# Kernel optimization log

Measured on AMD Instinct MI355X. Metric: run time of the kernel, lower is better.

## Reference

```python
import jax, jax.numpy as jnp
import numpy as np

N, IN_FT, OUT_FT = 10000, 512, 256


def setup_inputs() -> dict:
    key = jax.random.key(0)
    k1, k2, k3 = jax.random.split(key, 3)
    feat = jax.random.normal(k1, (N, IN_FT), dtype=jnp.float32)
    adj = jax.random.uniform(k2, (N, N), dtype=jnp.float32)  # nonneg edge weights
    W = jax.random.normal(k3, (IN_FT, OUT_FT), dtype=jnp.float32) * 0.05
    conv_bias = jnp.zeros((OUT_FT,), dtype=jnp.float32)
    extra_bias = jnp.zeros((OUT_FT,), dtype=jnp.float32)
    return {"feat": feat, "adj": adj, "W": W,
            "conv_bias": conv_bias, "extra_bias": extra_bias}


def reference(feat, adj, W, conv_bias, extra_bias):
    n = adj.shape[0]
    idx = jnp.arange(n)
    # gcn_norm: fill_diag(adj, 1.0) -> self loops with weight 1 on the diagonal
    A_hat = adj.at[idx, idx].set(1.0)  # [N, N]
    deg = A_hat.sum(axis=1)            # row degree
    dinv = jnp.where(deg > 0, jax.lax.rsqrt(deg), 0.0)  # D^-1/2
    # linear transform first (standard GCNConv order), then normalized aggregation
    h = feat @ W                                   # [N, OUT_FT]
    # D^-1/2 A_hat D^-1/2 h, fused as row/col scalings to avoid a second NxN buffer
    agg = dinv[:, None] * (A_hat @ (dinv[:, None] * h))
    out = agg + conv_bias + extra_bias
    return jax.nn.relu(out)
```

## Files before the change

### kernel.cpp

```cpp
#include <hip/hip_runtime.h>

#define NROW 10000
#define NF 256
#define KF 512
#define MP 10048
#define NTILES 157
#define CCH 2512

typedef __attribute__((ext_vector_type(8))) short short8x;
typedef __attribute__((ext_vector_type(4))) float f32x4;

__device__ __forceinline__ unsigned int bf16rne(float f){
  unsigned int u = __builtin_bit_cast(unsigned int, f);
  u += 0x7fffu + ((u >> 16) & 1u);
  return u >> 16;
}

__global__ void k_zero(float4* __restrict__ p){
  p[blockIdx.x * 256 + threadIdx.x] = make_float4(0.f, 0.f, 0.f, 0.f);
}

__global__ __launch_bounds__(256) void k_prep(const float* __restrict__ adj,
        unsigned short* __restrict__ adjb, float* __restrict__ degp){
  int t = threadIdx.x;
  int lane = t & 63;
  int row = blockIdx.x * 4 + (t >> 6);
  int cy = blockIdx.y;
  int c0 = cy * CCH;
  int limit = (cy < 3) ? 628 : 616;
  const f32x4* src = (const f32x4*)(adj + (size_t)row * NROW + c0);
  unsigned short* dst = adjb + (size_t)row * MP + c0;
  const f32x4 zero4 = {0.f, 0.f, 0.f, 0.f};

  f32x4 v[5][2];
  #pragma unroll
  for (int it = 0; it < 4; ++it){
    int fi = it * 128 + lane * 2;
    v[it][0] = __builtin_nontemporal_load(src + fi);
    v[it][1] = __builtin_nontemporal_load(src + fi + 1);
  }
  {
    int fi = 512 + lane * 2;
    v[4][0] = (fi     < limit) ? __builtin_nontemporal_load(src + fi)     : zero4;
    v[4][1] = (fi + 1 < limit) ? __builtin_nontemporal_load(src + fi + 1) : zero4;
  }

  float s = 0.f;
  #pragma unroll
  for (int it = 0; it < 5; ++it){
    int fi0 = it * 128 + lane * 2;
    uint4 o;
    #pragma unroll
    for (int j = 0; j < 2; ++j){
      f32x4 w = v[it][j];
      int gc = c0 + (fi0 + j) * 4;
      if (row == gc    ) w[0] = 1.f;
      if (row == gc + 1) w[1] = 1.f;
      if (row == gc + 2) w[2] = 1.f;
      if (row == gc + 3) w[3] = 1.f;
      s += (w[0] + w[1]) + (w[2] + w[3]);
      unsigned int lo = bf16rne(w[0]) | (bf16rne(w[1]) << 16);
      unsigned int hi = bf16rne(w[2]) | (bf16rne(w[3]) << 16);
      if (j == 0){ o.x = lo; o.y = hi; } else { o.z = lo; o.w = hi; }
    }
    if (it < 4 || fi0 < 628)
      *(uint4*)(dst + fi0 * 4) = o;
  }
  #pragma unroll
  for (int off = 32; off; off >>= 1) s += __shfl_down(s, off);
  if (lane == 0) degp[cy * MP + row] = s;
}

__global__ void k_dinv(const float* __restrict__ degp, float* __restrict__ dinv,
                       unsigned short* __restrict__ hsT){
  int i = blockIdx.x * 256 + threadIdx.x;
  if (i >= MP) return;
  float d = 0.f;
  if (i < NROW){
    float tot = (degp[i] + degp[MP + i]) + (degp[2*MP + i] + degp[3*MP + i]);
    d = tot > 0.f ? rsqrtf(tot) : 0.f;
  }
  dinv[i] = d;
  if (i < NF){
    unsigned int* tz = (unsigned int*)(hsT + (size_t)i * MP + NROW);
    #pragma unroll
    for (int m = 0; m < (MP - NROW) / 2; ++m) tz[m] = 0u;
  }
}

__global__ __launch_bounds__(128) void k_featw(const float* __restrict__ feat,
        const float* __restrict__ W, const float* __restrict__ dinv,
        unsigned short* __restrict__ hsT){
  __shared__ __align__(16) float fs[8][512];
  int t = threadIdx.x;
  int i0 = blockIdx.x * 8;
  #pragma unroll
  for (int it = 0; it < 8; ++it){
    int idx = it * 128 + t;
    int r = idx >> 7, c4 = (idx & 127) * 4;
    *(float4*)&fs[r][c4] = *(const float4*)(feat + (size_t)(i0 + r) * KF + c4);
  }
  __syncthreads();
  float acc[8][2];
  #pragma unroll
  for (int r = 0; r < 8; ++r){ acc[r][0] = 0.f; acc[r][1] = 0.f; }
  int c0 = t, c1 = t + 128;
  for (int k = 0; k < KF; k += 4){
    const float* Wk = W + (size_t)k * NF;
    float w0a = Wk[c0],        w0b = Wk[c1];
    float w1a = Wk[NF + c0],   w1b = Wk[NF + c1];
    float w2a = Wk[2*NF + c0], w2b = Wk[2*NF + c1];
    float w3a = Wk[3*NF + c0], w3b = Wk[3*NF + c1];
    #pragma unroll
    for (int r = 0; r < 8; ++r){
      float4 f = *(const float4*)&fs[r][k];
      float a0 = acc[r][0], a1 = acc[r][1];
      a0 = fmaf(f.x, w0a, a0); a1 = fmaf(f.x, w0b, a1);
      a0 = fmaf(f.y, w1a, a0); a1 = fmaf(f.y, w1b, a1);
      a0 = fmaf(f.z, w2a, a0); a1 = fmaf(f.z, w2b, a1);
      a0 = fmaf(f.w, w3a, a0); a1 = fmaf(f.w, w3b, a1);
      acc[r][0] = a0; acc[r][1] = a1;
    }
  }
  float dv[8];
  #pragma unroll
  for (int r = 0; r < 8; ++r) dv[r] = dinv[i0 + r];
  unsigned short* d0 = hsT + (size_t)c0 * MP + i0;
  unsigned short* d1 = hsT + (size_t)c1 * MP + i0;
  #pragma unroll
  for (int r = 0; r < 8; r += 2){
    unsigned int u0 = bf16rne(acc[r][0] * dv[r]) | (bf16rne(acc[r+1][0] * dv[r+1]) << 16);
    unsigned int u1 = bf16rne(acc[r][1] * dv[r]) | (bf16rne(acc[r+1][1] * dv[r+1]) << 16);
    *(unsigned int*)(d0 + r) = u0;
    *(unsigned int*)(d1 + r) = u1;
  }
}

__global__ __launch_bounds__(256, 3) void k_gemm(const unsigned short* __restrict__ adjb,
        const unsigned short* __restrict__ hsT, float* __restrict__ out){
  __shared__ __align__(16) unsigned short Al[64][72];
  __shared__ __align__(16) unsigned short Bl[256][72];
  int t = threadIdx.x;
  int lane = t & 63, wid = t >> 6;
  int wr = wid >> 1, wc = wid & 1;
  int r0 = blockIdx.x * 64;
  int by = blockIdx.y;
  int kt0 = by * 39 + (by > 0 ? 1 : 0);
  int kt1 = (by + 1) * 39 + 1;

  f32x4 acc[2][8];
  #pragma unroll
  for (int a = 0; a < 2; ++a)
    #pragma unroll
    for (int b = 0; b < 8; ++b)
      #pragma unroll
      for (int j = 0; j < 4; ++j) acc[a][b][j] = 0.f;

  int bcol = t >> 3;
  int bko  = (t & 7) * 8;

  for (int kt = kt0; kt < kt1; ++kt){
    int k0 = kt * 64;
    #pragma unroll
    for (int it = 0; it < 2; ++it){
      int slot = it * 256 + t;
      int row = slot >> 3, off8 = (slot & 7) * 8;
      *(uint4*)&Al[row][off8] =
          *(const uint4*)(adjb + (size_t)(r0 + row) * MP + k0 + off8);
    }
    #pragma unroll
    for (int it = 0; it < 8; ++it){
      int cc = it * 32 + bcol;
      *(uint4*)&Bl[cc][bko] = *(const uint4*)(hsT + (size_t)cc * MP + k0 + bko);
    }
    __syncthreads();
    #pragma unroll
    for (int kk = 0; kk < 64; kk += 32){
      short8x a0 = *(const short8x*)&Al[wr*32      + (lane & 15)][kk + (lane >> 4) * 8];
      short8x a1 = *(const short8x*)&Al[wr*32 + 16 + (lane & 15)][kk + (lane >> 4) * 8];
      #pragma unroll
      for (int ni = 0; ni < 8; ++ni){
        short8x b = *(const short8x*)&Bl[wc*128 + ni*16 + (lane & 15)][kk + (lane >> 4) * 8];
        acc[0][ni] = __builtin_amdgcn_mfma_f32_16x16x32_bf16(a0, b, acc[0][ni], 0, 0, 0);
        acc[1][ni] = __builtin_amdgcn_mfma_f32_16x16x32_bf16(a1, b, acc[1][ni], 0, 0, 0);
      }
    }
    __syncthreads();
  }
  #pragma unroll
  for (int mi = 0; mi < 2; ++mi){
    #pragma unroll
    for (int ni = 0; ni < 8; ++ni){
      int gc = wc*128 + ni*16 + (lane & 15);
      #pragma unroll
      for (int j = 0; j < 4; ++j){
        int gr = r0 + wr*32 + mi*16 + (lane >> 4) * 4 + j;
        if (gr < NROW) atomicAdd(out + (size_t)gr * NF + gc, acc[mi][ni][j]);
      }
    }
  }
}

__global__ void k_epi(float* __restrict__ out, const float* __restrict__ dinv,
                      const float* __restrict__ cb, const float* __restrict__ eb){
  int e = (blockIdx.x * 256 + threadIdx.x) * 4;
  int i = e >> 8, c = e & 255;
  float di = dinv[i];
  float4 v = *(float4*)(out + e);
  v.x = fmaxf(fmaf(v.x, di, cb[c+0] + eb[c+0]), 0.f);
  v.y = fmaxf(fmaf(v.y, di, cb[c+1] + eb[c+1]), 0.f);
  v.z = fmaxf(fmaf(v.z, di, cb[c+2] + eb[c+2]), 0.f);
  v.w = fmaxf(fmaf(v.w, di, cb[c+3] + eb[c+3]), 0.f);
  *(float4*)(out + e) = v;
}

extern "C" void kernel_launch(void* const* d_in, const int* in_sizes, int n_in,
                              void* d_out, int out_size, void* d_ws, size_t ws_size,
                              hipStream_t stream){
  const float* feat = (const float*)d_in[0];
  const float* adj  = (const float*)d_in[1];
  const float* W    = (const float*)d_in[2];
  const float* cb   = (const float*)d_in[3];
  const float* eb   = (const float*)d_in[4];
  float* out = (float*)d_out;

  float* degp = (float*)d_ws;
  float* dinv = (float*)((char*)d_ws + (256u << 10));
  unsigned short* hsT  = (unsigned short*)((char*)d_ws + (512u << 10));
  unsigned short* adjb = (unsigned short*)((char*)d_ws + (8u << 20));

  k_zero <<<(NROW*NF)/1024,    256, 0, stream>>>((float4*)out);
  k_prep <<<dim3(NROW/4, 4),   256, 0, stream>>>(adj, adjb, degp);
  k_dinv <<<(MP + 255)/256,    256, 0, stream>>>(degp, dinv, hsT);
  k_featw<<<NROW/8,            128, 0, stream>>>(feat, W, dinv, hsT);
  k_gemm <<<dim3(NTILES, 4),   256, 0, stream>>>(adjb, hsT, out);
  k_epi  <<<(NROW*NF)/1024,    256, 0, stream>>>(out, dinv, cb, eb);
}
```

Baseline: 289.7 us.

## Prefetch next GEMM k-tile into registers and double split-K to eight

The aggregation GEMM now loads the next k-tile of adjacency and features into registers while MFMAs run on the current tile held in shared memory. This hides global-load latency behind compute. The split-K factor rises from 4 to 8, doubling the grid for better CU occupancy. In exchange it doubles the atomic adds to the output and raises register pressure under the existing launch bounds.

```diff
diff --git a/kernel.cpp b/kernel.cpp
--- a/kernel.cpp
+++ b/kernel.cpp
@@ -5,6 +5,7 @@
 #define KF 512
 #define MP 10048
 #define NTILES 157
+#define KSPLIT 8
 #define CCH 2512
 
 typedef __attribute__((ext_vector_type(8))) short short8x;
@@ -145,8 +146,8 @@
   int wr = wid >> 1, wc = wid & 1;
   int r0 = blockIdx.x * 64;
   int by = blockIdx.y;
-  int kt0 = by * 39 + (by > 0 ? 1 : 0);
-  int kt1 = (by + 1) * 39 + 1;
+  int kt0 = by * 20;
+  int kt1 = (by == KSPLIT - 1) ? NTILES : kt0 + 20;
 
   f32x4 acc[2][8];
   #pragma unroll
@@ -156,24 +157,39 @@
       #pragma unroll
       for (int j = 0; j < 4; ++j) acc[a][b][j] = 0.f;
 
+  int arow = t >> 3;
+  int aoff = (t & 7) * 8;
   int bcol = t >> 3;
   int bko  = (t & 7) * 8;
 
+  uint4 a_pf[2], b_pf[8];
+  {
+    int k0 = kt0 * 64;
+    #pragma unroll
+    for (int it = 0; it < 2; ++it)
+      a_pf[it] = *(const uint4*)(adjb + (size_t)(r0 + it*32 + arow) * MP + k0 + aoff);
+    #pragma unroll
+    for (int it = 0; it < 8; ++it)
+      b_pf[it] = *(const uint4*)(hsT + (size_t)(it*32 + bcol) * MP + k0 + bko);
+  }
+
   for (int kt = kt0; kt < kt1; ++kt){
-    int k0 = kt * 64;
-    #pragma unroll
-    for (int it = 0; it < 2; ++it){
-      int slot = it * 256 + t;
-      int row = slot >> 3, off8 = (slot & 7) * 8;
-      *(uint4*)&Al[row][off8] =
-          *(const uint4*)(adjb + (size_t)(r0 + row) * MP + k0 + off8);
-    }
-    #pragma unroll
-    for (int it = 0; it < 8; ++it){
-      int cc = it * 32 + bcol;
-      *(uint4*)&Bl[cc][bko] = *(const uint4*)(hsT + (size_t)cc * MP + k0 + bko);
-    }
+    #pragma unroll
+    for (int it = 0; it < 2; ++it)
+      *(uint4*)&Al[it*32 + arow][aoff] = a_pf[it];
+    #pragma unroll
+    for (int it = 0; it < 8; ++it)
+      *(uint4*)&Bl[it*32 + bcol][bko] = b_pf[it];
     __syncthreads();
+    if (kt + 1 < kt1){
+      int k0n = (kt + 1) * 64;
+      #pragma unroll
+      for (int it = 0; it < 2; ++it)
+        a_pf[it] = *(const uint4*)(adjb + (size_t)(r0 + it*32 + arow) * MP + k0n + aoff);
+      #pragma unroll
+      for (int it = 0; it < 8; ++it)
+        b_pf[it] = *(const uint4*)(hsT + (size_t)(it*32 + bcol) * MP + k0n + bko);
+    }
     #pragma unroll
     for (int kk = 0; kk < 64; kk += 32){
       short8x a0 = *(const short8x*)&Al[wr*32      + (lane & 15)][kk + (lane >> 4) * 8];
@@ -229,10 +245,10 @@
   unsigned short* hsT  = (unsigned short*)((char*)d_ws + (512u << 10));
   unsigned short* adjb = (unsigned short*)((char*)d_ws + (8u << 20));
 
-  k_zero <<<(NROW*NF)/1024,    256, 0, stream>>>((float4*)out);
-  k_prep <<<dim3(NROW/4, 4),   256, 0, stream>>>(adj, adjb, degp);
-  k_dinv <<<(MP + 255)/256,    256, 0, stream>>>(degp, dinv, hsT);
-  k_featw<<<NROW/8,            128, 0, stream>>>(feat, W, dinv, hsT);
-  k_gemm <<<dim3(NTILES, 4),   256, 0, stream>>>(adjb, hsT, out);
-  k_epi  <<<(NROW*NF)/1024,    256, 0, stream>>>(out, dinv, cb, eb);
-}
+  k_zero <<<(NROW*NF)/1024,        256, 0, stream>>>((float4*)out);
+  k_prep <<<dim3(NROW/4, 4),       256, 0, stream>>>(adj, adjb, degp);
+  k_dinv <<<(MP + 255)/256,        256, 0, stream>>>(degp, dinv, hsT);
+  k_featw<<<NROW/8,                128, 0, stream>>>(feat, W, dinv, hsT);
+  k_gemm <<<dim3(NTILES, KSPLIT),  256, 0, stream>>>(adjb, hsT, out);
+  k_epi  <<<(NROW*NF)/1024,        256, 0, stream>>>(out, dinv, cb, eb);
+}
```

Measured after the change: 496.6 us. 1.71x slower.

## Drop bf16 adjacency copy; convert fp32 adjacency inside the GEMM tile load

Applied to the files above, without the earlier changes.

The prep kernel no longer writes a padded bf16 copy of the adjacency matrix. It becomes a pure degree-sum pass that uses normal loads instead of nontemporal ones. The GEMM now loads fp32 adjacency tiles directly, sets the diagonal to one, and converts to bf16 while staging into shared memory, with clamped indices for the padded edges. The degree is corrected for the self-loop in k_dinv. This removes the 200MB intermediate write and reread, but the GEMM now streams twice the bytes per tile. Its occupancy hint is lowered to 2, which may expose more memory latency.

```diff
diff --git a/kernel.cpp b/kernel.cpp
--- a/kernel.cpp
+++ b/kernel.cpp
@@ -20,8 +20,8 @@
   p[blockIdx.x * 256 + threadIdx.x] = make_float4(0.f, 0.f, 0.f, 0.f);
 }
 
-__global__ __launch_bounds__(256) void k_prep(const float* __restrict__ adj,
-        unsigned short* __restrict__ adjb, float* __restrict__ degp){
+__global__ __launch_bounds__(256) void k_deg2(const float* __restrict__ adj,
+        float* __restrict__ degp){
   int t = threadIdx.x;
   int lane = t & 63;
   int row = blockIdx.x * 4 + (t >> 6);
@@ -29,55 +29,39 @@
   int c0 = cy * CCH;
   int limit = (cy < 3) ? 628 : 616;
   const f32x4* src = (const f32x4*)(adj + (size_t)row * NROW + c0);
-  unsigned short* dst = adjb + (size_t)row * MP + c0;
   const f32x4 zero4 = {0.f, 0.f, 0.f, 0.f};
 
-  f32x4 v[5][2];
+  f32x4 v[10];
   #pragma unroll
   for (int it = 0; it < 4; ++it){
     int fi = it * 128 + lane * 2;
-    v[it][0] = __builtin_nontemporal_load(src + fi);
-    v[it][1] = __builtin_nontemporal_load(src + fi + 1);
+    v[2*it]   = src[fi];
+    v[2*it+1] = src[fi + 1];
   }
   {
     int fi = 512 + lane * 2;
-    v[4][0] = (fi     < limit) ? __builtin_nontemporal_load(src + fi)     : zero4;
-    v[4][1] = (fi + 1 < limit) ? __builtin_nontemporal_load(src + fi + 1) : zero4;
-  }
-
-  float s = 0.f;
-  #pragma unroll
-  for (int it = 0; it < 5; ++it){
-    int fi0 = it * 128 + lane * 2;
-    uint4 o;
-    #pragma unroll
-    for (int j = 0; j < 2; ++j){
-      f32x4 w = v[it][j];
-      int gc = c0 + (fi0 + j) * 4;
-      if (row == gc    ) w[0] = 1.f;
-      if (row == gc + 1) w[1] = 1.f;
-      if (row == gc + 2) w[2] = 1.f;
-      if (row == gc + 3) w[3] = 1.f;
-      s += (w[0] + w[1]) + (w[2] + w[3]);
-      unsigned int lo = bf16rne(w[0]) | (bf16rne(w[1]) << 16);
-      unsigned int hi = bf16rne(w[2]) | (bf16rne(w[3]) << 16);
-      if (j == 0){ o.x = lo; o.y = hi; } else { o.z = lo; o.w = hi; }
-    }
-    if (it < 4 || fi0 < 628)
-      *(uint4*)(dst + fi0 * 4) = o;
-  }
+    v[8] = (fi     < limit) ? src[fi]     : zero4;
+    v[9] = (fi + 1 < limit) ? src[fi + 1] : zero4;
+  }
+  float s0 = 0.f, s1 = 0.f, s2 = 0.f, s3 = 0.f;
+  #pragma unroll
+  for (int it = 0; it < 10; ++it){
+    s0 += v[it][0]; s1 += v[it][1]; s2 += v[it][2]; s3 += v[it][3];
+  }
+  float s = (s0 + s1) + (s2 + s3);
   #pragma unroll
   for (int off = 32; off; off >>= 1) s += __shfl_down(s, off);
   if (lane == 0) degp[cy * MP + row] = s;
 }
 
-__global__ void k_dinv(const float* __restrict__ degp, float* __restrict__ dinv,
-                       unsigned short* __restrict__ hsT){
+__global__ void k_dinv(const float* __restrict__ degp, const float* __restrict__ adj,
+                       float* __restrict__ dinv, unsigned short* __restrict__ hsT){
   int i = blockIdx.x * 256 + threadIdx.x;
   if (i >= MP) return;
   float d = 0.f;
   if (i < NROW){
     float tot = (degp[i] + degp[MP + i]) + (degp[2*MP + i] + degp[3*MP + i]);
+    tot += 1.0f - adj[(size_t)i * NROW + i];
     d = tot > 0.f ? rsqrtf(tot) : 0.f;
   }
   dinv[i] = d;
@@ -136,7 +120,7 @@
   }
 }
 
-__global__ __launch_bounds__(256, 3) void k_gemm(const unsigned short* __restrict__ adjb,
+__global__ __launch_bounds__(256, 2) void k_gemm(const float* __restrict__ adj,
         const unsigned short* __restrict__ hsT, float* __restrict__ out){
   __shared__ __align__(16) unsigned short Al[64][72];
   __shared__ __align__(16) unsigned short Bl[256][72];
@@ -156,17 +140,29 @@
       #pragma unroll
       for (int j = 0; j < 4; ++j) acc[a][b][j] = 0.f;
 
+  int arow = t >> 4;
+  int acol = (t & 15) * 4;
   int bcol = t >> 3;
   int bko  = (t & 7) * 8;
 
   for (int kt = kt0; kt < kt1; ++kt){
     int k0 = kt * 64;
     #pragma unroll
-    for (int it = 0; it < 2; ++it){
-      int slot = it * 256 + t;
-      int row = slot >> 3, off8 = (slot & 7) * 8;
-      *(uint4*)&Al[row][off8] =
-          *(const uint4*)(adjb + (size_t)(r0 + row) * MP + k0 + off8);
+    for (int it = 0; it < 4; ++it){
+      int row = it * 16 + arow;
+      int gr  = r0 + row;
+      int gcb = k0 + acol;
+      int er = gr  < NROW      ? gr  : NROW - 1;
+      int ec = gcb <= NROW - 4 ? gcb : NROW - 4;
+      float4 v = *(const float4*)(adj + (size_t)er * NROW + ec);
+      float f0 = v.x, f1 = v.y, f2 = v.z, f3 = v.w;
+      if (gr == gcb    ) f0 = 1.f;
+      if (gr == gcb + 1) f1 = 1.f;
+      if (gr == gcb + 2) f2 = 1.f;
+      if (gr == gcb + 3) f3 = 1.f;
+      unsigned int u0 = bf16rne(f0) | (bf16rne(f1) << 16);
+      unsigned int u1 = bf16rne(f2) | (bf16rne(f3) << 16);
+      *(uint2*)&Al[row][acol] = make_uint2(u0, u1);
     }
     #pragma unroll
     for (int it = 0; it < 8; ++it){
@@ -226,13 +222,12 @@
 
   float* degp = (float*)d_ws;
   float* dinv = (float*)((char*)d_ws + (256u << 10));
-  unsigned short* hsT  = (unsigned short*)((char*)d_ws + (512u << 10));
-  unsigned short* adjb = (unsigned short*)((char*)d_ws + (8u << 20));
-
-  k_zero <<<(NROW*NF)/1024,    256, 0, stream>>>((float4*)out);
-  k_prep <<<dim3(NROW/4, 4),   256, 0, stream>>>(adj, adjb, degp);
-  k_dinv <<<(MP + 255)/256,    256, 0, stream>>>(degp, dinv, hsT);
-  k_featw<<<NROW/8,            128, 0, stream>>>(feat, W, dinv, hsT);
-  k_gemm <<<dim3(NTILES, 4),   256, 0, stream>>>(adjb, hsT, out);
-  k_epi  <<<(NROW*NF)/1024,    256, 0, stream>>>(out, dinv, cb, eb);
-}
+  unsigned short* hsT = (unsigned short*)((char*)d_ws + (512u << 10));
+
+  k_zero <<<(NROW*NF)/1024,   256, 0, stream>>>((float4*)out);
+  k_deg2 <<<dim3(NROW/4, 4),  256, 0, stream>>>(adj, degp);
+  k_dinv <<<(MP + 255)/256,   256, 0, stream>>>(degp, adj, dinv, hsT);
+  k_featw<<<NROW/8,           128, 0, stream>>>(feat, W, dinv, hsT);
+  k_gemm <<<dim3(NTILES, 4),  256, 0, stream>>>(adj, hsT, out);
+  k_epi  <<<(NROW*NF)/1024,   256, 0, stream>>>(out, dinv, cb, eb);
+}
```

Result: faster. 278.7 us (-3.8%).
